# Kernel tuning notes

Hardware: AMD Instinct MI355X
Metric: run time of the kernel (lower is better)

Reference implementation:

```python
import jax, jax.numpy as jnp
import numpy as np
import math

VOCAB, D, L, B, S = 32000, 1024, 6, 4, 1024
FF = 4 * D


def sinusoidal_pe(max_len, d_model):
    pos = np.arange(max_len)[:, None].astype(np.float32)
    div = np.exp(np.arange(0, d_model, 2).astype(np.float32) * (-math.log(10000.0) / d_model))
    pe = np.zeros((max_len, d_model), dtype=np.float32)
    pe[:, 0::2] = np.sin(pos * div)
    pe[:, 1::2] = np.cos(pos * div)
    return jnp.asarray(pe)


def layernorm(x, g, b, eps=1e-5):
    mu = jnp.mean(x, axis=-1, keepdims=True)
    var = jnp.mean(jnp.square(x - mu), axis=-1, keepdims=True)
    return (x - mu) * jax.lax.rsqrt(var + eps) * g + b


def setup_inputs() -> dict:
    key = jax.random.key(0)
    ks = jax.random.split(key, 16)
    s = 0.02
    inp = {
        "input_ids": jax.random.randint(ks[0], (B, S), 0, VOCAB, dtype=jnp.int32),
        "attention_mask": jnp.ones((B, S), dtype=jnp.int32),
        "emb": jax.random.normal(ks[1], (VOCAB, D), jnp.float32) * s,
        "Wq": jax.random.normal(ks[2], (L, D, D), jnp.float32) * s,
        "Wk": jax.random.normal(ks[3], (L, D, D), jnp.float32) * s,
        "Wv": jax.random.normal(ks[4], (L, D, D), jnp.float32) * s,
        "bq": jnp.zeros((L, D), jnp.float32),
        "bk": jnp.zeros((L, D), jnp.float32),
        "bv": jnp.zeros((L, D), jnp.float32),
        "g1": jnp.ones((L, D), jnp.float32),
        "beta1": jnp.zeros((L, D), jnp.float32),
        "Wf1": jax.random.normal(ks[5], (L, D, FF), jnp.float32) * s,
        "bf1": jnp.zeros((L, FF), jnp.float32),
        "Wf2": jax.random.normal(ks[6], (L, FF, D), jnp.float32) * s,
        "bf2": jnp.zeros((L, D), jnp.float32),
        "g2": jnp.ones((L, D), jnp.float32),
        "beta2": jnp.zeros((L, D), jnp.float32),
    }
    return inp


def reference(input_ids, attention_mask, emb, Wq, Wk, Wv, bq, bk, bv,
              g1, beta1, Wf1, bf1, Wf2, bf2, g2, beta2):
    pe = sinusoidal_pe(1024, D)
    x = emb[input_ids] + pe[: input_ids.shape[1]]           # [B,S,D]
    mask = (attention_mask[:, None, :] != 0)                # [B,1,S]
    scale = 1.0 / math.sqrt(D)
    for l in range(L):
        Q = jnp.einsum('bsd,de->bse', x, Wq[l]) + bq[l]
        K = jnp.einsum('bsd,de->bse', x, Wk[l]) + bk[l]
        V = jnp.einsum('bsd,de->bse', x, Wv[l]) + bv[l]
        scores = jnp.einsum('bqd,bkd->bqk', Q, K) * scale   # [B,S,S]
        scores = jnp.where(mask, scores, -1e9)
        attn = jax.nn.softmax(scores, axis=-1)
        a = jnp.einsum('bqk,bkd->bqd', attn, V)
        x = layernorm(x + a, g1[l], beta1[l])
        h = jax.nn.relu(jnp.einsum('bsd,df->bsf', x, Wf1[l]) + bf1[l])
        f = jnp.einsum('bsf,fd->bsd', h, Wf2[l]) + bf2[l]
        x = layernorm(x + f, g2[l], beta2[l])
    return x
```

## Files before the change

### kernel.cpp

```cpp
#include <hip/hip_runtime.h>

typedef __bf16 bf16_t;
typedef __bf16 bf16x8 __attribute__((ext_vector_type(8)));
typedef float f32x4 __attribute__((ext_vector_type(4)));
typedef unsigned short u16;

#define DEV static __device__ __forceinline__

DEV float bf2f(u16 u) { __bf16 h = __builtin_bit_cast(__bf16, u); return (float)h; }
DEV u16 f2bf(float f) { __bf16 h = (__bf16)f; return __builtin_bit_cast(u16, h); }

DEV void gll16(bf16_t* lds, const bf16_t* g) {
    __builtin_amdgcn_global_load_lds(
        (const __attribute__((address_space(1))) void*)g,
        (__attribute__((address_space(3))) void*)lds, 16, 0, 0);
}

#define WAITV(N) asm volatile("s_waitcnt vmcnt(" #N ")" ::: "memory")

template <int EPI>
__global__ __launch_bounds__(512, 1)
void gemm8p(const bf16_t* __restrict__ A, int lda,
            const bf16_t* __restrict__ Bt, int ldb,
            bf16_t* __restrict__ C, int ldc,
            const float* __restrict__ bias, int K,
            long kadv, long cadv)
{
    __shared__ bf16_t Asm[2 * 2 * 8192];
    __shared__ bf16_t Bsm[2 * 2 * 8192];
    const int tid = threadIdx.x, w = tid >> 6, l = tid & 63;
    const int z = blockIdx.z;
    A  += (size_t)z * kadv;
    Bt += (size_t)z * kadv;
    C  += (size_t)z * cadv;

    const int gx = gridDim.x;
    int lin = blockIdx.y * gx + blockIdx.x;
    const int nlin = gx * gridDim.y;
    lin = (lin & 7) * (nlin >> 3) + (lin >> 3);
    const size_t row0 = (size_t)(lin / gx) * 256;
    const size_t col0 = (size_t)(lin % gx) * 256;

    const int wr = w >> 2, wc = w & 3;
    const int bh = wc >> 1;
    const int browoff = (wc & 1) * 64;
    const int fr = l & 15, q = l >> 4, sw = l & 7;

    const int srow = w * 8 + (l >> 3);
    const int sslot8 = ((l & 7) ^ ((l >> 3) & 7)) * 8;
    const bf16_t* AgH0 = A  + (row0 + srow) * (size_t)lda + sslot8;
    const bf16_t* BgH0 = Bt + (col0 + srow) * (size_t)ldb + sslot8;
    const size_t a128 = (size_t)128 * lda, b128 = (size_t)128 * ldb;
    const size_t a64  = (size_t)64 * lda,  b64  = (size_t)64 * ldb;
    const int wlds = w * 512;

#define STAGE_PAIR(buf, tt, p)                                                 \
    do {                                                                       \
        const int koff = (tt) * 64;                                            \
        if ((p) == 0) {                                                        \
            gll16(Asm + ((buf)*2+0)*8192 + wlds,        AgH0 + koff);          \
            gll16(Asm + ((buf)*2+0)*8192 + 4096 + wlds, AgH0 + koff + a64);    \
        } else if ((p) == 1) {                                                 \
            gll16(Asm + ((buf)*2+1)*8192 + wlds,        AgH0 + a128 + koff);   \
            gll16(Asm + ((buf)*2+1)*8192 + 4096 + wlds, AgH0 + a128 + koff + a64); \
        } else if ((p) == 2) {                                                 \
            gll16(Bsm + ((buf)*2+0)*8192 + wlds,        BgH0 + koff);          \
            gll16(Bsm + ((buf)*2+0)*8192 + 4096 + wlds, BgH0 + koff + b64);    \
        } else {                                                               \
            gll16(Bsm + ((buf)*2+1)*8192 + wlds,        BgH0 + b128 + koff);   \
            gll16(Bsm + ((buf)*2+1)*8192 + 4096 + wlds, BgH0 + b128 + koff + b64); \
        }                                                                      \
    } while (0)

    f32x4 acc[8][4] = {};
    const int NT = K >> 6;

    STAGE_PAIR(0, 0, 0); STAGE_PAIR(0, 0, 1); STAGE_PAIR(0, 0, 2); STAGE_PAIR(0, 0, 3);
    if (NT > 1) { STAGE_PAIR(1, 1, 0); WAITV(2); } else { WAITV(0); }
    __builtin_amdgcn_sched_barrier(0);
    __builtin_amdgcn_s_barrier();

    bf16x8 aR[4][2], bR[4][2];
    for (int t = 0; t < NT; ++t) {
        const int cur = t & 1, nxt = cur ^ 1;
        const bool hasN1 = (t + 1 < NT), hasN2 = (t + 2 < NT);
        const bf16_t* Ab = Asm + (cur * 2 + wr) * 8192;
        const bf16_t* Bb = Bsm + (cur * 2 + bh) * 8192;

#pragma unroll
        for (int mi = 0; mi < 4; mi++)
#pragma unroll
            for (int kk = 0; kk < 2; kk++)
                aR[mi][kk] = *(const bf16x8*)&Ab[(mi * 16 + fr) * 64 + ((kk * 4 + q) ^ sw) * 8];
#pragma unroll
        for (int ni = 0; ni < 2; ni++)
#pragma unroll
            for (int kk = 0; kk < 2; kk++)
                bR[ni][kk] = *(const bf16x8*)&Bb[(browoff + ni * 16 + fr) * 64 + ((kk * 4 + q) ^ sw) * 8];
        if (hasN1) STAGE_PAIR(nxt, t + 1, 1);
        __builtin_amdgcn_s_barrier();
        __builtin_amdgcn_s_setprio(1);
#pragma unroll
        for (int mi = 0; mi < 4; mi++)
#pragma unroll
            for (int ni = 0; ni < 2; ni++)
#pragma unroll
                for (int kk = 0; kk < 2; kk++)
                    acc[mi][ni] = __builtin_amdgcn_mfma_f32_16x16x32_bf16(aR[mi][kk], bR[ni][kk], acc[mi][ni], 0, 0, 0);
        __builtin_amdgcn_s_setprio(0);
        __builtin_amdgcn_s_barrier();

#pragma unroll
        for (int ni = 2; ni < 4; ni++)
#pragma unroll
            for (int kk = 0; kk < 2; kk++)
                bR[ni][kk] = *(const bf16x8*)&Bb[(browoff + ni * 16 + fr) * 64 + ((kk * 4 + q) ^ sw) * 8];
        if (hasN1) STAGE_PAIR(nxt, t + 1, 2);
        __builtin_amdgcn_s_barrier();
        __builtin_amdgcn_s_setprio(1);
#pragma unroll
        for (int mi = 0; mi < 4; mi++)
#pragma unroll
            for (int ni = 2; ni < 4; ni++)
#pragma unroll
                for (int kk = 0; kk < 2; kk++)
                    acc[mi][ni] = __builtin_amdgcn_mfma_f32_16x16x32_bf16(aR[mi][kk], bR[ni][kk], acc[mi][ni], 0, 0, 0);
        __builtin_amdgcn_s_setprio(0);
        __builtin_amdgcn_s_barrier();

#pragma unroll
        for (int mi = 0; mi < 4; mi++)
#pragma unroll
            for (int kk = 0; kk < 2; kk++)
                aR[mi][kk] = *(const bf16x8*)&Ab[((4 + mi) * 16 + fr) * 64 + ((kk * 4 + q) ^ sw) * 8];
        if (hasN1) STAGE_PAIR(nxt, t + 1, 3);
        __builtin_amdgcn_s_barrier();
        __builtin_amdgcn_s_setprio(1);
#pragma unroll
        for (int mi = 0; mi < 4; mi++)
#pragma unroll
            for (int ni = 0; ni < 2; ni++)
#pragma unroll
                for (int kk = 0; kk < 2; kk++)
                    acc[4 + mi][ni] = __builtin_amdgcn_mfma_f32_16x16x32_bf16(aR[mi][kk], bR[ni][kk], acc[4 + mi][ni], 0, 0, 0);
        __builtin_amdgcn_s_setprio(0);
        __builtin_amdgcn_s_barrier();

        if (hasN2) STAGE_PAIR(cur, t + 2, 0);
        __builtin_amdgcn_s_setprio(1);
#pragma unroll
        for (int mi = 0; mi < 4; mi++)
#pragma unroll
            for (int ni = 2; ni < 4; ni++)
#pragma unroll
                for (int kk = 0; kk < 2; kk++)
                    acc[4 + mi][ni] = __builtin_amdgcn_mfma_f32_16x16x32_bf16(aR[mi][kk], bR[ni][kk], acc[4 + mi][ni], 0, 0, 0);
        __builtin_amdgcn_s_setprio(0);
        if (hasN1) {
            if (hasN2) { WAITV(2); } else { WAITV(0); }
            __builtin_amdgcn_sched_barrier(0);
        }
        __builtin_amdgcn_s_barrier();
    }
#undef STAGE_PAIR

    const int cr = q * 4, cc = fr;
#pragma unroll
    for (int ni = 0; ni < 4; ni++) {
        size_t c = col0 + wc * 64 + ni * 16 + cc;
        float bv = bias ? bias[c] : 0.f;
#pragma unroll
        for (int mi = 0; mi < 8; mi++) {
            size_t r = row0 + wr * 128 + mi * 16 + cr;
#pragma unroll
            for (int j = 0; j < 4; j++) {
                float v = acc[mi][ni][j] + bv;
                if (EPI == 1) v = fmaxf(v, 0.f);
                C[(r + j) * ldc + c] = (bf16_t)v;
            }
        }
    }
}

template <int EPI>
__global__ __launch_bounds__(256)
void gemm_db(const bf16_t* __restrict__ A, int lda, long sA,
             const bf16_t* __restrict__ Bt, int ldb, long sB,
             void* __restrict__ Cv, int ldc, long sC,
             const float* __restrict__ bias, int K, float scale)
{
    __shared__ bf16_t Asm[2][128 * 64];
    __shared__ bf16_t Bsm[2][128 * 64];
    const int tid = threadIdx.x, w = tid >> 6, l = tid & 63;
    const int bz = blockIdx.z;

    const int gx = gridDim.x;
    int lin = blockIdx.y * gx + blockIdx.x;
    const int nlin = gx * gridDim.y;
    lin = (lin & 7) * (nlin >> 3) + (lin >> 3);
    const size_t row0 = (size_t)(lin / gx) * 128;
    const size_t col0 = (size_t)(lin % gx) * 128;

    A  += (size_t)bz * sA;
    Bt += (size_t)bz * sB;

    const int lr = l >> 3;
    const int sl = (l & 7) ^ lr;
    const bf16_t* Ag = A  + (row0 + (size_t)(w * 32) + lr) * lda + sl * 8;
    const bf16_t* Bg = Bt + (col0 + (size_t)(w * 32) + lr) * ldb + sl * 8;
    const int wlds = (w * 32) * 64;

#define STA(buf, tt)                                                           \
    do { const int ko = (tt) * 64;                                             \
        _Pragma("unroll")                                                      \
        for (int c = 0; c < 4; c++)                                            \
            gll16(&Asm[buf][wlds + c * 8 * 64], Ag + (size_t)(c * 8) * lda + ko); \
    } while (0)
#define STB(buf, tt)                                                           \
    do { const int ko = (tt) * 64;                                             \
        _Pragma("unroll")                                                      \
        for (int c = 0; c < 4; c++)                                            \
            gll16(&Bsm[buf][wlds + c * 8 * 64], Bg + (size_t)(c * 8) * ldb + ko); \
    } while (0)

    const int wm = (w >> 1) * 64, wn = (w & 1) * 64;
    const int fr16 = l & 15, q4 = l >> 4, sw = l & 7;
    f32x4 acc[4][4] = {};
    const int NT = K >> 6;

    STA(0, 0); STB(0, 0);
    if (NT > 1) { STA(1, 1); WAITV(4); } else { WAITV(0); }
    __builtin_amdgcn_sched_barrier(0);
    __builtin_amdgcn_s_barrier();

    for (int t = 0; t < NT; ++t) {
        const int cur = t & 1, nxt = cur ^ 1;
        const bool hasN1 = (t + 1 < NT), hasN2 = (t + 2 < NT);

        bf16x8 a0[4], b0[4];
#pragma unroll
        for (int i = 0; i < 4; i++) {
            const int slot = (q4 ^ sw) * 8;
            a0[i] = *(const bf16x8*)&Asm[cur][(wm + i * 16 + fr16) * 64 + slot];
            b0[i] = *(const bf16x8*)&Bsm[cur][(wn + i * 16 + fr16) * 64 + slot];
        }
        if (hasN1) STB(nxt, t + 1);
        __builtin_amdgcn_s_barrier();
        __builtin_amdgcn_s_setprio(1);
#pragma unroll
        for (int mi = 0; mi < 4; mi++)
#pragma unroll
            for (int ni = 0; ni < 4; ni++)
                acc[mi][ni] = __builtin_amdgcn_mfma_f32_16x16x32_bf16(a0[mi], b0[ni], acc[mi][ni], 0, 0, 0);
        __builtin_amdgcn_s_setprio(0);
        __builtin_amdgcn_s_barrier();

        bf16x8 a1[4], b1[4];
#pragma unroll
        for (int i = 0; i < 4; i++) {
            const int slot = ((4 + q4) ^ sw) * 8;
            a1[i] = *(const bf16x8*)&Asm[cur][(wm + i * 16 + fr16) * 64 + slot];
            b1[i] = *(const bf16x8*)&Bsm[cur][(wn + i * 16 + fr16) * 64 + slot];
        }
        __builtin_amdgcn_s_barrier();
        __builtin_amdgcn_s_setprio(1);
#pragma unroll
        for (int mi = 0; mi < 4; mi++)
#pragma unroll
            for (int ni = 0; ni < 4; ni++)
                acc[mi][ni] = __builtin_amdgcn_mfma_f32_16x16x32_bf16(a1[mi], b1[ni], acc[mi][ni], 0, 0, 0);
        __builtin_amdgcn_s_setprio(0);
        if (hasN2) STA(cur, t + 2);
        if (hasN1) {
            if (hasN2) { WAITV(4); } else { WAITV(0); }
            __builtin_amdgcn_sched_barrier(0);
        }
        __builtin_amdgcn_s_barrier();
    }
#undef STA
#undef STB

    const int cr = q4 * 4, cc = fr16;
    if (EPI == 2) {
        float* C = (float*)Cv + (size_t)bz * sC;
#pragma unroll
        for (int mi = 0; mi < 4; mi++)
#pragma unroll
            for (int ni = 0; ni < 4; ni++) {
                size_t r = row0 + wm + mi * 16 + cr;
                size_t c = col0 + wn + ni * 16 + cc;
#pragma unroll
                for (int j = 0; j < 4; j++)
                    C[(r + j) * ldc + c] = acc[mi][ni][j] * scale;
            }
    } else {
        bf16_t* C = (bf16_t*)Cv + (size_t)bz * sC;
#pragma unroll
        for (int ni = 0; ni < 4; ni++) {
            size_t c = col0 + wn + ni * 16 + cc;
            float bv = bias ? bias[c] : 0.f;
#pragma unroll
            for (int mi = 0; mi < 4; mi++) {
                size_t r = row0 + wm + mi * 16 + cr;
#pragma unroll
                for (int j = 0; j < 4; j++) {
                    float v = acc[mi][ni][j] + bv;
                    if (EPI == 1) v = fmaxf(v, 0.f);
                    C[(r + j) * ldc + c] = (bf16_t)v;
                }
            }
        }
    }
}

__global__ __launch_bounds__(256)
void transpose_f32_bf16(const float* __restrict__ in, bf16_t* __restrict__ out,
                        int ldin, int ldout, long sin_, long sout_)
{
    __shared__ bf16_t t[64][72];
    in  += (size_t)blockIdx.z * sin_;
    out += (size_t)blockIdx.z * sout_;
    const int bx = blockIdx.x * 64;
    const int by = blockIdx.y * 64;
    const int tid = threadIdx.x;
    const int cj = (tid & 15) * 4, ri = tid >> 4;
#pragma unroll
    for (int k = 0; k < 4; k++) {
        int r = ri + k * 16;
        float4 v = *(const float4*)&in[(size_t)(by + r) * ldin + bx + cj];
        ushort4 o = {f2bf(v.x), f2bf(v.y), f2bf(v.z), f2bf(v.w)};
        *(ushort4*)&t[r][cj] = o;
    }
    __syncthreads();
#pragma unroll
    for (int k = 0; k < 4; k++) {
        int i = ri + k * 16;
        ushort4 o;
        o.x = __builtin_bit_cast(u16, t[cj + 0][i]);
        o.y = __builtin_bit_cast(u16, t[cj + 1][i]);
        o.z = __builtin_bit_cast(u16, t[cj + 2][i]);
        o.w = __builtin_bit_cast(u16, t[cj + 3][i]);
        *(ushort4*)&out[(size_t)(bx + i) * ldout + by + cj] = o;
    }
}

__global__ __launch_bounds__(256)
void transpose_bf16(const bf16_t* __restrict__ in, bf16_t* __restrict__ out,
                    int ldin, int ldout, long sin_, long sout_)
{
    __shared__ bf16_t t[64][72];
    in  += (size_t)blockIdx.z * sin_;
    out += (size_t)blockIdx.z * sout_;
    const int bx = blockIdx.x * 64;
    const int by = blockIdx.y * 64;
    const int tid = threadIdx.x;
    const int cj = (tid & 15) * 4, ri = tid >> 4;
#pragma unroll
    for (int k = 0; k < 4; k++) {
        int r = ri + k * 16;
        *(ushort4*)&t[r][cj] = *(const ushort4*)&in[(size_t)(by + r) * ldin + bx + cj];
    }
    __syncthreads();
#pragma unroll
    for (int k = 0; k < 4; k++) {
        int i = ri + k * 16;
        ushort4 o;
        o.x = __builtin_bit_cast(u16, t[cj + 0][i]);
        o.y = __builtin_bit_cast(u16, t[cj + 1][i]);
        o.z = __builtin_bit_cast(u16, t[cj + 2][i]);
        o.w = __builtin_bit_cast(u16, t[cj + 3][i]);
        *(ushort4*)&out[(size_t)(bx + i) * ldout + by + cj] = o;
    }
}

__global__ __launch_bounds__(256)
void embed_kernel(const int* __restrict__ ids, const float* __restrict__ emb,
                  float* __restrict__ x, bf16_t* __restrict__ xb)
{
    const int row = blockIdx.x;
    const int s = row & 1023;
    const int id = ids[row];
    const float* er = emb + (size_t)id * 1024;
    float* xr = x + (size_t)row * 1024;
    bf16_t* br = xb + (size_t)row * 1024;
#pragma unroll
    for (int k = 0; k < 2; k++) {
        int i = threadIdx.x + 256 * k;
        int d = 2 * i;
        float dv = expf((float)d * -0.008994473019508f);
        float ph = (float)s * dv;
        float sv, cv;
        sincosf(ph, &sv, &cv);
        float2 ev = *(const float2*)&er[d];
        float x0 = ev.x + sv;
        float x1 = ev.y + cv;
        float2 xo = {x0, x1};
        *(float2*)&xr[d] = xo;
        ushort2 bo = {f2bf(x0), f2bf(x1)};
        *(ushort2*)&br[d] = bo;
    }
}

__global__ __launch_bounds__(256)
void softmax_kernel(const float* __restrict__ sc, const int* __restrict__ amask,
                    bf16_t* __restrict__ p)
{
    const int row = blockIdx.x * 4 + (threadIdx.x >> 6);
    const int l = threadIdx.x & 63;
    const int b = row >> 10;
    const float* s = sc + (size_t)row * 1024;
    const int* m = amask + (size_t)b * 1024;
    float v[16];
    float mx = -3.0e38f;
#pragma unroll
    for (int i = 0; i < 4; i++) {
        int c = 4 * l + 256 * i;
        float4 sv = *(const float4*)&s[c];
        int4 mv = *(const int4*)&m[c];
        v[4 * i + 0] = mv.x ? sv.x : -1e9f;
        v[4 * i + 1] = mv.y ? sv.y : -1e9f;
        v[4 * i + 2] = mv.z ? sv.z : -1e9f;
        v[4 * i + 3] = mv.w ? sv.w : -1e9f;
        mx = fmaxf(mx, fmaxf(fmaxf(v[4 * i], v[4 * i + 1]), fmaxf(v[4 * i + 2], v[4 * i + 3])));
    }
#pragma unroll
    for (int o = 32; o; o >>= 1) mx = fmaxf(mx, __shfl_xor(mx, o, 64));
    float sum = 0.f;
#pragma unroll
    for (int i = 0; i < 16; i++) { v[i] = __expf(v[i] - mx); sum += v[i]; }
#pragma unroll
    for (int o = 32; o; o >>= 1) sum += __shfl_xor(sum, o, 64);
    float inv = 1.0f / sum;
#pragma unroll
    for (int i = 0; i < 4; i++) {
        int c = 4 * l + 256 * i;
        ushort4 st;
        st.x = f2bf(v[4 * i + 0] * inv);
        st.y = f2bf(v[4 * i + 1] * inv);
        st.z = f2bf(v[4 * i + 2] * inv);
        st.w = f2bf(v[4 * i + 3] * inv);
        *(ushort4*)&p[(size_t)row * 1024 + c] = st;
    }
}

__global__ __launch_bounds__(256)
void ln_kernel(const float* __restrict__ xin, const bf16_t* __restrict__ add,
               const float* __restrict__ g, const float* __restrict__ beta,
               float* __restrict__ xout, bf16_t* __restrict__ bout)
{
    __shared__ float red[8];
    const int row = blockIdx.x;
    const int t = threadIdx.x;
    const size_t base = (size_t)row * 1024 + t * 4;
    float4 xv = *(const float4*)&xin[base];
    ushort4 au = *(const ushort4*)&add[base];
    float tv[4];
    tv[0] = xv.x + bf2f(au.x);
    tv[1] = xv.y + bf2f(au.y);
    tv[2] = xv.z + bf2f(au.z);
    tv[3] = xv.w + bf2f(au.w);
    float s = tv[0] + tv[1] + tv[2] + tv[3];
    float s2 = tv[0] * tv[0] + tv[1] * tv[1] + tv[2] * tv[2] + tv[3] * tv[3];
#pragma unroll
    for (int o = 32; o; o >>= 1) { s += __shfl_xor(s, o, 64); s2 += __shfl_xor(s2, o, 64); }
    if ((t & 63) == 0) { red[t >> 6] = s; red[4 + (t >> 6)] = s2; }
    __syncthreads();
    s = red[0] + red[1] + red[2] + red[3];
    s2 = red[4] + red[5] + red[6] + red[7];
    const float mu = s * (1.f / 1024.f);
    const float var = s2 * (1.f / 1024.f) - mu * mu;
    const float rs = rsqrtf(var + 1e-5f);
    float4 gu = *(const float4*)&g[t * 4];
    float4 bu = *(const float4*)&beta[t * 4];
    float y0 = (tv[0] - mu) * rs * gu.x + bu.x;
    float y1 = (tv[1] - mu) * rs * gu.y + bu.y;
    float y2 = (tv[2] - mu) * rs * gu.z + bu.z;
    float y3 = (tv[3] - mu) * rs * gu.w + bu.w;
    float4 yo = {y0, y1, y2, y3};
    *(float4*)&xout[base] = yo;
    ushort4 ob = {f2bf(y0), f2bf(y1), f2bf(y2), f2bf(y3)};
    *(ushort4*)&bout[base] = ob;
}

__global__ __launch_bounds__(256)
void ln4_kernel(const float* __restrict__ xin, const bf16_t* __restrict__ p,
                long pstride, const float* __restrict__ fbias,
                const float* __restrict__ g, const float* __restrict__ beta,
                float* __restrict__ xout, bf16_t* __restrict__ bout)
{
    __shared__ float red[8];
    const int row = blockIdx.x;
    const int t = threadIdx.x;
    const size_t base = (size_t)row * 1024 + t * 4;
    float4 xv = *(const float4*)&xin[base];
    float4 bb = *(const float4*)&fbias[t * 4];
    float tv[4] = {xv.x + bb.x, xv.y + bb.y, xv.z + bb.z, xv.w + bb.w};
#pragma unroll
    for (int z = 0; z < 4; z++) {
        ushort4 au = *(const ushort4*)&p[(size_t)z * pstride + base];
        tv[0] += bf2f(au.x); tv[1] += bf2f(au.y);
        tv[2] += bf2f(au.z); tv[3] += bf2f(au.w);
    }
    float s = tv[0] + tv[1] + tv[2] + tv[3];
    float s2 = tv[0] * tv[0] + tv[1] * tv[1] + tv[2] * tv[2] + tv[3] * tv[3];
#pragma unroll
    for (int o = 32; o; o >>= 1) { s += __shfl_xor(s, o, 64); s2 += __shfl_xor(s2, o, 64); }
    if ((t & 63) == 0) { red[t >> 6] = s; red[4 + (t >> 6)] = s2; }
    __syncthreads();
    s = red[0] + red[1] + red[2] + red[3];
    s2 = red[4] + red[5] + red[6] + red[7];
    const float mu = s * (1.f / 1024.f);
    const float var = s2 * (1.f / 1024.f) - mu * mu;
    const float rs = rsqrtf(var + 1e-5f);
    float4 gu = *(const float4*)&g[t * 4];
    float4 bu = *(const float4*)&beta[t * 4];
    float y0 = (tv[0] - mu) * rs * gu.x + bu.x;
    float y1 = (tv[1] - mu) * rs * gu.y + bu.y;
    float y2 = (tv[2] - mu) * rs * gu.z + bu.z;
    float y3 = (tv[3] - mu) * rs * gu.w + bu.w;
    float4 yo = {y0, y1, y2, y3};
    *(float4*)&xout[base] = yo;
    ushort4 ob = {f2bf(y0), f2bf(y1), f2bf(y2), f2bf(y3)};
    *(ushort4*)&bout[base] = ob;
}

__global__ __launch_bounds__(256)
void biascat6_kernel(const float* __restrict__ bq, const float* __restrict__ bk,
                     const float* __restrict__ bv, float* __restrict__ o)
{
    int i = blockIdx.x * 256 + threadIdx.x;
    int lyr = i / 3072, j = i - lyr * 3072;
    o[i] = (j < 1024) ? bq[lyr * 1024 + j]
         : (j < 2048) ? bk[lyr * 1024 + j - 1024]
                      : bv[lyr * 1024 + j - 2048];
}


extern "C" void kernel_launch(void* const* d_in, const int* in_sizes, int n_in,
                              void* d_out, int out_size, void* d_ws, size_t ws_size,
                              hipStream_t stream)
{
    const int*   ids = (const int*)d_in[0];
    const int*   am  = (const int*)d_in[1];
    const float* emb = (const float*)d_in[2];
    const float* Wq  = (const float*)d_in[3];
    const float* Wk  = (const float*)d_in[4];
    const float* Wv  = (const float*)d_in[5];
    const float* bq  = (const float*)d_in[6];
    const float* bk  = (const float*)d_in[7];
    const float* bv  = (const float*)d_in[8];
    const float* g1  = (const float*)d_in[9];
    const float* be1 = (const float*)d_in[10];
    const float* Wf1 = (const float*)d_in[11];
    const float* bf1 = (const float*)d_in[12];
    const float* Wf2 = (const float*)d_in[13];
    const float* bf2_ = (const float*)d_in[14];
    const float* g2  = (const float*)d_in[15];
    const float* be2 = (const float*)d_in[16];

    char* ws = (char*)d_ws;
    float*  x      = (float*)(ws);
    bf16_t* xb     = (bf16_t*)(ws + (16LL << 20));
    bf16_t* qkv    = (bf16_t*)(ws + (24LL << 20));
    bf16_t* vt     = (bf16_t*)(ws + (48LL << 20));
    bf16_t* fpart  = (bf16_t*)(ws + (24LL << 20));
    float*  scores = (float*)(ws + (56LL << 20));
    bf16_t* p      = (bf16_t*)(ws + (72LL << 20));
    bf16_t* h      = (bf16_t*)(ws + (56LL << 20));
    bf16_t* attn   = (bf16_t*)(ws + (88LL << 20));
    bf16_t* wqkvTA = (bf16_t*)(ws + (96LL << 20));
    bf16_t* wf1TA  = (bf16_t*)(ws + (132LL << 20));
    bf16_t* wf2TA  = (bf16_t*)(ws + (180LL << 20));
    float*  qbiasA = (float*)(ws + (228LL << 20));

    const size_t DD = 1024 * 1024;

    transpose_f32_bf16<<<dim3(16, 16, 6), 256, 0, stream>>>(Wq, wqkvTA,          1024, 1024, (long)DD, 3L * DD);
    transpose_f32_bf16<<<dim3(16, 16, 6), 256, 0, stream>>>(Wk, wqkvTA + DD,     1024, 1024, (long)DD, 3L * DD);
    transpose_f32_bf16<<<dim3(16, 16, 6), 256, 0, stream>>>(Wv, wqkvTA + 2 * DD, 1024, 1024, (long)DD, 3L * DD);
    transpose_f32_bf16<<<dim3(64, 16, 6), 256, 0, stream>>>(Wf1, wf1TA, 4096, 1024, 4L * DD, 4L * DD);
    transpose_f32_bf16<<<dim3(16, 64, 6), 256, 0, stream>>>(Wf2, wf2TA, 1024, 4096, 4L * DD, 4L * DD);
    biascat6_kernel<<<72, 256, 0, stream>>>(bq, bk, bv, qbiasA);

    embed_kernel<<<4096, 256, 0, stream>>>(ids, emb, x, xb);

    for (int l = 0; l < 6; l++) {
        gemm8p<0><<<dim3(12, 16, 1), 512, 0, stream>>>(xb, 1024, wqkvTA + (size_t)l * 3 * DD, 1024,
                                                       qkv, 3072, qbiasA + l * 3072, 1024, 0, 0);
        transpose_bf16<<<dim3(16, 16, 4), 256, 0, stream>>>(qkv + 2048, vt, 3072, 1024,
                                                            1024L * 3072, 1024L * 1024);
        gemm_db<2><<<dim3(8, 8, 4), 256, 0, stream>>>(qkv, 3072, 1024L * 3072,
                                                      qkv + 1024, 3072, 1024L * 3072,
                                                      scores, 1024, 1024L * 1024,
                                                      nullptr, 1024, 0.03125f);
        softmax_kernel<<<1024, 256, 0, stream>>>(scores, am, p);
        gemm_db<0><<<dim3(8, 8, 4), 256, 0, stream>>>(p, 1024, 1024L * 1024,
                                                      vt, 1024, 1024L * 1024,
                                                      attn, 1024, 1024L * 1024,
                                                      nullptr, 1024, 0.f);
        ln_kernel<<<4096, 256, 0, stream>>>(x, attn, g1 + l * 1024, be1 + l * 1024, x, xb);
        gemm8p<1><<<dim3(16, 16, 1), 512, 0, stream>>>(xb, 1024, wf1TA + (size_t)l * 4 * DD, 1024,
                                                       h, 4096, bf1 + l * 4096, 1024, 0, 0);
        gemm8p<0><<<dim3(4, 16, 4), 512, 0, stream>>>(h, 4096, wf2TA + (size_t)l * 4 * DD, 4096,
                                                      fpart, 1024, nullptr, 1024,
                                                      1024, 4096L * 1024);
        float* xo = (l == 5) ? (float*)d_out : x;
        ln4_kernel<<<4096, 256, 0, stream>>>(x, fpart, 4096L * 1024, bf2_ + l * 1024,
                                             g2 + l * 1024, be2 + l * 1024, xo, xb);
    }
    (void)in_sizes; (void)n_in; (void)out_size; (void)ws_size;
}
```

Measured before the change: 1.352 ms.

## Cut GEMM inner-loop barriers and merge prep and softmax/V-transpose launches

The 8-wave GEMM main loop drops from four barrier-separated sub-phases to two. It loads all B fragments at once and issues three of the four next-tile stage pairs up front, which needs more registers but cuts s_barrier stalls. The double-buffered GEMM removes three of its four per-iteration barriers and keeps only the one before restaging the current buffer. Separately, the weight transposes, bias concat and embedding are merged into one prep kernel, and the V transpose is folded into the softmax launch, to reduce launch overhead and idle gaps.

```diff
diff --git a/kernel.cpp b/kernel.cpp
--- a/kernel.cpp
+++ b/kernel.cpp
@@ -80,82 +80,53 @@
     __builtin_amdgcn_sched_barrier(0);
     __builtin_amdgcn_s_barrier();
 
-    bf16x8 aR[4][2], bR[4][2];
     for (int t = 0; t < NT; ++t) {
         const int cur = t & 1, nxt = cur ^ 1;
         const bool hasN1 = (t + 1 < NT), hasN2 = (t + 2 < NT);
         const bf16_t* Ab = Asm + (cur * 2 + wr) * 8192;
         const bf16_t* Bb = Bsm + (cur * 2 + bh) * 8192;
 
+        bf16x8 aR[4][2], bR[4][2];
 #pragma unroll
         for (int mi = 0; mi < 4; mi++)
 #pragma unroll
             for (int kk = 0; kk < 2; kk++)
                 aR[mi][kk] = *(const bf16x8*)&Ab[(mi * 16 + fr) * 64 + ((kk * 4 + q) ^ sw) * 8];
 #pragma unroll
-        for (int ni = 0; ni < 2; ni++)
+        for (int ni = 0; ni < 4; ni++)
 #pragma unroll
             for (int kk = 0; kk < 2; kk++)
                 bR[ni][kk] = *(const bf16x8*)&Bb[(browoff + ni * 16 + fr) * 64 + ((kk * 4 + q) ^ sw) * 8];
-        if (hasN1) STAGE_PAIR(nxt, t + 1, 1);
-        __builtin_amdgcn_s_barrier();
+        if (hasN1) { STAGE_PAIR(nxt, t + 1, 1); STAGE_PAIR(nxt, t + 1, 2); }
         __builtin_amdgcn_s_setprio(1);
 #pragma unroll
         for (int mi = 0; mi < 4; mi++)
 #pragma unroll
-            for (int ni = 0; ni < 2; ni++)
+            for (int ni = 0; ni < 4; ni++)
 #pragma unroll
                 for (int kk = 0; kk < 2; kk++)
                     acc[mi][ni] = __builtin_amdgcn_mfma_f32_16x16x32_bf16(aR[mi][kk], bR[ni][kk], acc[mi][ni], 0, 0, 0);
         __builtin_amdgcn_s_setprio(0);
+
+        bf16x8 a2[4][2];
+#pragma unroll
+        for (int mi = 0; mi < 4; mi++)
+#pragma unroll
+            for (int kk = 0; kk < 2; kk++)
+                a2[mi][kk] = *(const bf16x8*)&Ab[((4 + mi) * 16 + fr) * 64 + ((kk * 4 + q) ^ sw) * 8];
+        if (hasN1) STAGE_PAIR(nxt, t + 1, 3);
+        __builtin_amdgcn_s_setprio(1);
+#pragma unroll
+        for (int mi = 0; mi < 4; mi++)
+#pragma unroll
+            for (int ni = 0; ni < 4; ni++)
+#pragma unroll
+                for (int kk = 0; kk < 2; kk++)
+                    acc[4 + mi][ni] = __builtin_amdgcn_mfma_f32_16x16x32_bf16(a2[mi][kk], bR[ni][kk], acc[4 + mi][ni], 0, 0, 0);
+        __builtin_amdgcn_s_setprio(0);
+
         __builtin_amdgcn_s_barrier();
-
-#pragma unroll
-        for (int ni = 2; ni < 4; ni++)
-#pragma unroll
-            for (int kk = 0; kk < 2; kk++)
-                bR[ni][kk] = *(const bf16x8*)&Bb[(browoff + ni * 16 + fr) * 64 + ((kk * 4 + q) ^ sw) * 8];
-        if (hasN1) STAGE_PAIR(nxt, t + 1, 2);
-        __builtin_amdgcn_s_barrier();
-        __builtin_amdgcn_s_setprio(1);
-#pragma unroll
-        for (int mi = 0; mi < 4; mi++)
-#pragma unroll
-            for (int ni = 2; ni < 4; ni++)
-#pragma unroll
-                for (int kk = 0; kk < 2; kk++)
-                    acc[mi][ni] = __builtin_amdgcn_mfma_f32_16x16x32_bf16(aR[mi][kk], bR[ni][kk], acc[mi][ni], 0, 0, 0);
-        __builtin_amdgcn_s_setprio(0);
-        __builtin_amdgcn_s_barrier();
-
-#pragma unroll
-        for (int mi = 0; mi < 4; mi++)
-#pragma unroll
-            for (int kk = 0; kk < 2; kk++)
-                aR[mi][kk] = *(const bf16x8*)&Ab[((4 + mi) * 16 + fr) * 64 + ((kk * 4 + q) ^ sw) * 8];
-        if (hasN1) STAGE_PAIR(nxt, t + 1, 3);
-        __builtin_amdgcn_s_barrier();
-        __builtin_amdgcn_s_setprio(1);
-#pragma unroll
-        for (int mi = 0; mi < 4; mi++)
-#pragma unroll
-            for (int ni = 0; ni < 2; ni++)
-#pragma unroll
-                for (int kk = 0; kk < 2; kk++)
-                    acc[4 + mi][ni] = __builtin_amdgcn_mfma_f32_16x16x32_bf16(aR[mi][kk], bR[ni][kk], acc[4 + mi][ni], 0, 0, 0);
-        __builtin_amdgcn_s_setprio(0);
-        __builtin_amdgcn_s_barrier();
-
         if (hasN2) STAGE_PAIR(cur, t + 2, 0);
-        __builtin_amdgcn_s_setprio(1);
-#pragma unroll
-        for (int mi = 0; mi < 4; mi++)
-#pragma unroll
-            for (int ni = 2; ni < 4; ni++)
-#pragma unroll
-                for (int kk = 0; kk < 2; kk++)
-                    acc[4 + mi][ni] = __builtin_amdgcn_mfma_f32_16x16x32_bf16(aR[mi][kk], bR[ni][kk], acc[4 + mi][ni], 0, 0, 0);
-        __builtin_amdgcn_s_setprio(0);
         if (hasN1) {
             if (hasN2) { WAITV(2); } else { WAITV(0); }
             __builtin_amdgcn_sched_barrier(0);
@@ -237,15 +208,14 @@
         const int cur = t & 1, nxt = cur ^ 1;
         const bool hasN1 = (t + 1 < NT), hasN2 = (t + 2 < NT);
 
-        bf16x8 a0[4], b0[4];
+        bf16x8 a0[4], b0[4], a1[4], b1[4];
+        const int s0 = (q4 ^ sw) * 8, s1 = ((4 + q4) ^ sw) * 8;
 #pragma unroll
         for (int i = 0; i < 4; i++) {
-            const int slot = (q4 ^ sw) * 8;
-            a0[i] = *(const bf16x8*)&Asm[cur][(wm + i * 16 + fr16) * 64 + slot];
-            b0[i] = *(const bf16x8*)&Bsm[cur][(wn + i * 16 + fr16) * 64 + slot];
+            a0[i] = *(const bf16x8*)&Asm[cur][(wm + i * 16 + fr16) * 64 + s0];
+            b0[i] = *(const bf16x8*)&Bsm[cur][(wn + i * 16 + fr16) * 64 + s0];
         }
         if (hasN1) STB(nxt, t + 1);
-        __builtin_amdgcn_s_barrier();
         __builtin_amdgcn_s_setprio(1);
 #pragma unroll
         for (int mi = 0; mi < 4; mi++)
@@ -253,16 +223,11 @@
             for (int ni = 0; ni < 4; ni++)
                 acc[mi][ni] = __builtin_amdgcn_mfma_f32_16x16x32_bf16(a0[mi], b0[ni], acc[mi][ni], 0, 0, 0);
         __builtin_amdgcn_s_setprio(0);
-        __builtin_amdgcn_s_barrier();
-
-        bf16x8 a1[4], b1[4];
 #pragma unroll
         for (int i = 0; i < 4; i++) {
-            const int slot = ((4 + q4) ^ sw) * 8;
-            a1[i] = *(const bf16x8*)&Asm[cur][(wm + i * 16 + fr16) * 64 + slot];
-            b1[i] = *(const bf16x8*)&Bsm[cur][(wn + i * 16 + fr16) * 64 + slot];
-        }
-        __builtin_amdgcn_s_barrier();
+            a1[i] = *(const bf16x8*)&Asm[cur][(wm + i * 16 + fr16) * 64 + s1];
+            b1[i] = *(const bf16x8*)&Bsm[cur][(wn + i * 16 + fr16) * 64 + s1];
+        }
         __builtin_amdgcn_s_setprio(1);
 #pragma unroll
         for (int mi = 0; mi < 4; mi++)
@@ -270,6 +235,8 @@
             for (int ni = 0; ni < 4; ni++)
                 acc[mi][ni] = __builtin_amdgcn_mfma_f32_16x16x32_bf16(a1[mi], b1[ni], acc[mi][ni], 0, 0, 0);
         __builtin_amdgcn_s_setprio(0);
+
+        __builtin_amdgcn_s_barrier();
         if (hasN2) STA(cur, t + 2);
         if (hasN1) {
             if (hasN2) { WAITV(4); } else { WAITV(0); }
@@ -314,73 +281,71 @@
 }
 
 __global__ __launch_bounds__(256)
-void transpose_f32_bf16(const float* __restrict__ in, bf16_t* __restrict__ out,
-                        int ldin, int ldout, long sin_, long sout_)
-{
-    __shared__ bf16_t t[64][72];
-    in  += (size_t)blockIdx.z * sin_;
-    out += (size_t)blockIdx.z * sout_;
-    const int bx = blockIdx.x * 64;
-    const int by = blockIdx.y * 64;
-    const int tid = threadIdx.x;
-    const int cj = (tid & 15) * 4, ri = tid >> 4;
-#pragma unroll
-    for (int k = 0; k < 4; k++) {
-        int r = ri + k * 16;
-        float4 v = *(const float4*)&in[(size_t)(by + r) * ldin + bx + cj];
-        ushort4 o = {f2bf(v.x), f2bf(v.y), f2bf(v.z), f2bf(v.w)};
-        *(ushort4*)&t[r][cj] = o;
-    }
-    __syncthreads();
-#pragma unroll
-    for (int k = 0; k < 4; k++) {
-        int i = ri + k * 16;
-        ushort4 o;
-        o.x = __builtin_bit_cast(u16, t[cj + 0][i]);
-        o.y = __builtin_bit_cast(u16, t[cj + 1][i]);
-        o.z = __builtin_bit_cast(u16, t[cj + 2][i]);
-        o.w = __builtin_bit_cast(u16, t[cj + 3][i]);
-        *(ushort4*)&out[(size_t)(bx + i) * ldout + by + cj] = o;
-    }
-}
-
-__global__ __launch_bounds__(256)
-void transpose_bf16(const bf16_t* __restrict__ in, bf16_t* __restrict__ out,
-                    int ldin, int ldout, long sin_, long sout_)
-{
-    __shared__ bf16_t t[64][72];
-    in  += (size_t)blockIdx.z * sin_;
-    out += (size_t)blockIdx.z * sout_;
-    const int bx = blockIdx.x * 64;
-    const int by = blockIdx.y * 64;
-    const int tid = threadIdx.x;
-    const int cj = (tid & 15) * 4, ri = tid >> 4;
-#pragma unroll
-    for (int k = 0; k < 4; k++) {
-        int r = ri + k * 16;
-        *(ushort4*)&t[r][cj] = *(const ushort4*)&in[(size_t)(by + r) * ldin + bx + cj];
-    }
-    __syncthreads();
-#pragma unroll
-    for (int k = 0; k < 4; k++) {
-        int i = ri + k * 16;
-        ushort4 o;
-        o.x = __builtin_bit_cast(u16, t[cj + 0][i]);
-        o.y = __builtin_bit_cast(u16, t[cj + 1][i]);
-        o.z = __builtin_bit_cast(u16, t[cj + 2][i]);
-        o.w = __builtin_bit_cast(u16, t[cj + 3][i]);
-        *(ushort4*)&out[(size_t)(bx + i) * ldout + by + cj] = o;
-    }
-}
-
-__global__ __launch_bounds__(256)
-void embed_kernel(const int* __restrict__ ids, const float* __restrict__ emb,
-                  float* __restrict__ x, bf16_t* __restrict__ xb)
-{
-    const int row = blockIdx.x;
+void prep_kernel(const float* __restrict__ Wq, const float* __restrict__ Wk,
+                 const float* __restrict__ Wv, const float* __restrict__ Wf1,
+                 const float* __restrict__ Wf2,
+                 const float* __restrict__ bq, const float* __restrict__ bk,
+                 const float* __restrict__ bv,
+                 const int* __restrict__ ids, const float* __restrict__ emb,
+                 bf16_t* __restrict__ wqkvTA, bf16_t* __restrict__ wf1TA,
+                 bf16_t* __restrict__ wf2TA, float* __restrict__ qbiasA,
+                 float* __restrict__ x, bf16_t* __restrict__ xb)
+{
+    __shared__ bf16_t tls[64][72];
+    const size_t DD = 1024 * 1024;
+    int id = blockIdx.x;
+    if (id < 16896) {
+        const float* src; bf16_t* dst; int ldin, ldout, bx, by;
+        if (id < 4608) {
+            int layer = id / 768, r = id % 768, which = r >> 8, t = r & 255;
+            src = (which == 0 ? Wq : which == 1 ? Wk : Wv) + (size_t)layer * DD;
+            dst = wqkvTA + (size_t)layer * 3 * DD + (size_t)which * DD;
+            ldin = 1024; ldout = 1024; bx = (t & 15) * 64; by = (t >> 4) * 64;
+        } else if (id < 10752) {
+            int i = id - 4608, layer = i >> 10, t = i & 1023;
+            src = Wf1 + (size_t)layer * 4 * DD; dst = wf1TA + (size_t)layer * 4 * DD;
+            ldin = 4096; ldout = 1024; bx = (t & 63) * 64; by = (t >> 6) * 64;
+        } else {
+            int i = id - 10752, layer = i >> 10, t = i & 1023;
+            src = Wf2 + (size_t)layer * 4 * DD; dst = wf2TA + (size_t)layer * 4 * DD;
+            ldin = 1024; ldout = 4096; bx = (t & 15) * 64; by = (t >> 4) * 64;
+        }
+        const int tid = threadIdx.x;
+        const int cj = (tid & 15) * 4, ri = tid >> 4;
+#pragma unroll
+        for (int k = 0; k < 4; k++) {
+            int r = ri + k * 16;
+            float4 v = *(const float4*)&src[(size_t)(by + r) * ldin + bx + cj];
+            ushort4 o = {f2bf(v.x), f2bf(v.y), f2bf(v.z), f2bf(v.w)};
+            *(ushort4*)&tls[r][cj] = o;
+        }
+        __syncthreads();
+#pragma unroll
+        for (int k = 0; k < 4; k++) {
+            int i2 = ri + k * 16;
+            ushort4 o;
+            o.x = __builtin_bit_cast(u16, tls[cj + 0][i2]);
+            o.y = __builtin_bit_cast(u16, tls[cj + 1][i2]);
+            o.z = __builtin_bit_cast(u16, tls[cj + 2][i2]);
+            o.w = __builtin_bit_cast(u16, tls[cj + 3][i2]);
+            *(ushort4*)&dst[(size_t)(bx + i2) * ldout + by + cj] = o;
+        }
+        return;
+    }
+    id -= 16896;
+    if (id < 72) {
+        int i = id * 256 + threadIdx.x;
+        int lyr = i / 3072, j = i - lyr * 3072;
+        qbiasA[i] = (j < 1024) ? bq[lyr * 1024 + j]
+                  : (j < 2048) ? bk[lyr * 1024 + j - 1024]
+                               : bv[lyr * 1024 + j - 2048];
+        return;
+    }
+    id -= 72;
+    const int row = id;
     const int s = row & 1023;
-    const int id = ids[row];
-    const float* er = emb + (size_t)id * 1024;
+    const int eid = ids[row];
+    const float* er = emb + (size_t)eid * 1024;
     float* xr = x + (size_t)row * 1024;
     bf16_t* br = xb + (size_t)row * 1024;
 #pragma unroll
@@ -402,44 +367,73 @@
 }
 
 __global__ __launch_bounds__(256)
-void softmax_kernel(const float* __restrict__ sc, const int* __restrict__ amask,
-                    bf16_t* __restrict__ p)
-{
-    const int row = blockIdx.x * 4 + (threadIdx.x >> 6);
-    const int l = threadIdx.x & 63;
-    const int b = row >> 10;
-    const float* s = sc + (size_t)row * 1024;
-    const int* m = amask + (size_t)b * 1024;
-    float v[16];
-    float mx = -3.0e38f;
-#pragma unroll
-    for (int i = 0; i < 4; i++) {
-        int c = 4 * l + 256 * i;
-        float4 sv = *(const float4*)&s[c];
-        int4 mv = *(const int4*)&m[c];
-        v[4 * i + 0] = mv.x ? sv.x : -1e9f;
-        v[4 * i + 1] = mv.y ? sv.y : -1e9f;
-        v[4 * i + 2] = mv.z ? sv.z : -1e9f;
-        v[4 * i + 3] = mv.w ? sv.w : -1e9f;
-        mx = fmaxf(mx, fmaxf(fmaxf(v[4 * i], v[4 * i + 1]), fmaxf(v[4 * i + 2], v[4 * i + 3])));
-    }
-#pragma unroll
-    for (int o = 32; o; o >>= 1) mx = fmaxf(mx, __shfl_xor(mx, o, 64));
-    float sum = 0.f;
-#pragma unroll
-    for (int i = 0; i < 16; i++) { v[i] = __expf(v[i] - mx); sum += v[i]; }
-#pragma unroll
-    for (int o = 32; o; o >>= 1) sum += __shfl_xor(sum, o, 64);
-    float inv = 1.0f / sum;
-#pragma unroll
-    for (int i = 0; i < 4; i++) {
-        int c = 4 * l + 256 * i;
-        ushort4 st;
-        st.x = f2bf(v[4 * i + 0] * inv);
-        st.y = f2bf(v[4 * i + 1] * inv);
-        st.z = f2bf(v[4 * i + 2] * inv);
-        st.w = f2bf(v[4 * i + 3] * inv);
-        *(ushort4*)&p[(size_t)row * 1024 + c] = st;
+void softvt_kernel(const float* __restrict__ sc, const int* __restrict__ amask,
+                   bf16_t* __restrict__ p, const bf16_t* __restrict__ qkv,
+                   bf16_t* __restrict__ vt)
+{
+    __shared__ bf16_t tls[64][72];
+    int bid = blockIdx.x;
+    if (bid < 1024) {
+        const int row = bid * 4 + (threadIdx.x >> 6);
+        const int l = threadIdx.x & 63;
+        const int b = row >> 10;
+        const float* s = sc + (size_t)row * 1024;
+        const int* m = amask + (size_t)b * 1024;
+        float v[16];
+        float mx = -3.0e38f;
+#pragma unroll
+        for (int i = 0; i < 4; i++) {
+            int c = 4 * l + 256 * i;
+            float4 sv = *(const float4*)&s[c];
+            int4 mv = *(const int4*)&m[c];
+            v[4 * i + 0] = mv.x ? sv.x : -1e9f;
+            v[4 * i + 1] = mv.y ? sv.y : -1e9f;
+            v[4 * i + 2] = mv.z ? sv.z : -1e9f;
+            v[4 * i + 3] = mv.w ? sv.w : -1e9f;
+            mx = fmaxf(mx, fmaxf(fmaxf(v[4 * i], v[4 * i + 1]), fmaxf(v[4 * i + 2], v[4 * i + 3])));
+        }
+#pragma unroll
+        for (int o = 32; o; o >>= 1) mx = fmaxf(mx, __shfl_xor(mx, o, 64));
+        float sum = 0.f;
+#pragma unroll
+        for (int i = 0; i < 16; i++) { v[i] = __expf(v[i] - mx); sum += v[i]; }
+#pragma unroll
+        for (int o = 32; o; o >>= 1) sum += __shfl_xor(sum, o, 64);
+        float inv = 1.0f / sum;
+#pragma unroll
+        for (int i = 0; i < 4; i++) {
+            int c = 4 * l + 256 * i;
+            ushort4 st;
+            st.x = f2bf(v[4 * i + 0] * inv);
+            st.y = f2bf(v[4 * i + 1] * inv);
+            st.z = f2bf(v[4 * i + 2] * inv);
+            st.w = f2bf(v[4 * i + 3] * inv);
+            *(ushort4*)&p[(size_t)row * 1024 + c] = st;
+        }
+        return;
+    }
+    bid -= 1024;
+    const int z = bid >> 8, t = bid & 255;
+    const bf16_t* in = qkv + 2048 + (size_t)z * 1024 * 3072;
+    bf16_t* out = vt + (size_t)z * 1024 * 1024;
+    const int bx = (t & 15) * 64, by = (t >> 4) * 64;
+    const int tid = threadIdx.x;
+    const int cj = (tid & 15) * 4, ri = tid >> 4;
+#pragma unroll
+    for (int k = 0; k < 4; k++) {
+        int r = ri + k * 16;
+        *(ushort4*)&tls[r][cj] = *(const ushort4*)&in[(size_t)(by + r) * 3072 + bx + cj];
+    }
+    __syncthreads();
+#pragma unroll
+    for (int k = 0; k < 4; k++) {
+        int i2 = ri + k * 16;
+        ushort4 o;
+        o.x = __builtin_bit_cast(u16, tls[cj + 0][i2]);
+        o.y = __builtin_bit_cast(u16, tls[cj + 1][i2]);
+        o.z = __builtin_bit_cast(u16, tls[cj + 2][i2]);
+        o.w = __builtin_bit_cast(u16, tls[cj + 3][i2]);
+        *(ushort4*)&out[(size_t)(bx + i2) * 1024 + by + cj] = o;
     }
 }
 
@@ -524,17 +518,6 @@
     *(ushort4*)&bout[base] = ob;
 }
 
-__global__ __launch_bounds__(256)
-void biascat6_kernel(const float* __restrict__ bq, const float* __restrict__ bk,
-                     const float* __restrict__ bv, float* __restrict__ o)
-{
-    int i = blockIdx.x * 256 + threadIdx.x;
-    int lyr = i / 3072, j = i - lyr * 3072;
-    o[i] = (j < 1024) ? bq[lyr * 1024 + j]
-         : (j < 2048) ? bk[lyr * 1024 + j - 1024]
-                      : bv[lyr * 1024 + j - 2048];
-}
-
 
 extern "C" void kernel_launch(void* const* d_in, const int* in_sizes, int n_in,
                               void* d_out, int out_size, void* d_ws, size_t ws_size,
@@ -575,25 +558,17 @@
 
     const size_t DD = 1024 * 1024;
 
-    transpose_f32_bf16<<<dim3(16, 16, 6), 256, 0, stream>>>(Wq, wqkvTA,          1024, 1024, (long)DD, 3L * DD);
-    transpose_f32_bf16<<<dim3(16, 16, 6), 256, 0, stream>>>(Wk, wqkvTA + DD,     1024, 1024, (long)DD, 3L * DD);
-    transpose_f32_bf16<<<dim3(16, 16, 6), 256, 0, stream>>>(Wv, wqkvTA + 2 * DD, 1024, 1024, (long)DD, 3L * DD);
-    transpose_f32_bf16<<<dim3(64, 16, 6), 256, 0, stream>>>(Wf1, wf1TA, 4096, 1024, 4L * DD, 4L * DD);
-    transpose_f32_bf16<<<dim3(16, 64, 6), 256, 0, stream>>>(Wf2, wf2TA, 1024, 4096, 4L * DD, 4L * DD);
-    biascat6_kernel<<<72, 256, 0, stream>>>(bq, bk, bv, qbiasA);
-
-    embed_kernel<<<4096, 256, 0, stream>>>(ids, emb, x, xb);
+    prep_kernel<<<21064, 256, 0, stream>>>(Wq, Wk, Wv, Wf1, Wf2, bq, bk, bv,
+                                           ids, emb, wqkvTA, wf1TA, wf2TA, qbiasA, x, xb);
 
     for (int l = 0; l < 6; l++) {
         gemm8p<0><<<dim3(12, 16, 1), 512, 0, stream>>>(xb, 1024, wqkvTA + (size_t)l * 3 * DD, 1024,
                                                        qkv, 3072, qbiasA + l * 3072, 1024, 0, 0);
-        transpose_bf16<<<dim3(16, 16, 4), 256, 0, stream>>>(qkv + 2048, vt, 3072, 1024,
-                                                            1024L * 3072, 1024L * 1024);
         gemm_db<2><<<dim3(8, 8, 4), 256, 0, stream>>>(qkv, 3072, 1024L * 3072,
                                                       qkv + 1024, 3072, 1024L * 3072,
                                                       scores, 1024, 1024L * 1024,
                                                       nullptr, 1024, 0.03125f);
-        softmax_kernel<<<1024, 256, 0, stream>>>(scores, am, p);
+        softvt_kernel<<<2048, 256, 0, stream>>>(scores, am, p, qkv, vt);
         gemm_db<0><<<dim3(8, 8, 4), 256, 0, stream>>>(p, 1024, 1024L * 1024,
                                                       vt, 1024, 1024L * 1024,
                                                       attn, 1024, 1024L * 1024,
```

New measurement: 1.274 ms. 1.06x faster.
